# Optimization experiments

Measured on AMD Instinct MI355X. Metric: run time of the kernel, lower is better.

## Reference

```python
import jax, jax.numpy as jnp
import numpy as np

GRID = 256          # number of block rows/cols (shape[0] == shape[1])
BS = 256            # block size == shape[1] in SparseAdjacency
K = 3               # kernel_size (odd)
HK = K // 2
BATCH = 4
FEAT = 256


def _connectivity(bs, k):
    # banded binary matrix: ones on diagonals -k//2..k//2 (SparseAdjacency connectivity)
    c = jnp.zeros((bs, bs), dtype=jnp.float32)
    for d in range(-(k // 2), k // 2 + 1):
        c = c + jnp.diag(jnp.ones(bs - abs(d), dtype=jnp.float32), d)
    return c


def setup_inputs() -> dict:
    key = jax.random.key(0)
    x = jax.random.normal(key, (BATCH, GRID * BS, FEAT), dtype=jnp.float32)
    # SparseAdjacency stores K identical banded connectivity blocks
    conn = _connectivity(BS, K)
    blocks = jnp.stack([conn] * K, axis=0)  # [K, BS, BS]
    return {"x": x, "blocks": blocks}


def reference(x, blocks):
    # Block-banded BCSR matmul: out_block[i] = sum_{d=-HK..HK} blocks[d+HK] @ x_block[i+d]
    # (clipped at boundaries -> zero padding), exactly the ptr/indices/data pattern
    # built by SparseAdjacency and consumed by SemiRegSpraseBCSR.matmul.
    B, NNbs, F = x.shape
    k, bs, _ = blocks.shape
    hk = k // 2
    n = NNbs // bs
    xb = x.reshape(B, n, bs, F)
    out = jnp.zeros_like(xb)
    for d in range(-hk, hk + 1):
        if d >= 0:
            shifted = jnp.pad(xb[:, d:], ((0, 0), (0, d), (0, 0), (0, 0)))
        else:
            shifted = jnp.pad(xb[:, :d], ((0, 0), (-d, 0), (0, 0), (0, 0)))
        # [bs,bs] @ [B,n,bs,F] -> [B,n,bs,F]
        out = out + jnp.einsum('ij,bnjf->bnif', blocks[d + hk], shifted)
    return out.reshape(B, NNbs, F)
```

## Files before the change

kernel.cpp:

```cpp
#include <hip/hip_runtime.h>


#define NB   256
#define BS   256
#define F4   64
#define RPT  8
#define TY   4
#define ROWS_PER_WG (RPT * TY)
#define CHUNKS (BS / ROWS_PER_WG)

typedef float f32x4 __attribute__((ext_vector_type(4)));

__global__ __launch_bounds__(256)
void blockconv_kernel(const float* __restrict__ x,
                      const float* __restrict__ w,
                      float* __restrict__ out)
{
    const int tx = threadIdx.x;
    const int ty = threadIdx.y;
    const int wg = blockIdx.x;

    const int chunk = wg & (CHUNKS - 1);
    const int n     = (wg >> 3) & (NB - 1);
    const int b     = wg >> 11;

    const int i_base = chunk * ROWS_PER_WG + ty * RPT;
    const int jlo    = i_base - 1;
    const int jlo_cl = jlo < 0 ? 0 : jlo;
    const bool lo_ok = (jlo >= 0);
    const bool hi_ok = (jlo + RPT + 1) < BS;

    const f32x4* __restrict__ x4 = (const f32x4*)x;
    f32x4* __restrict__ out4     = (f32x4*)out;

    f32x4 acc[RPT];
#pragma unroll
    for (int i = 0; i < RPT; ++i) acc[i] = (f32x4)(0.f);

#pragma unroll
    for (int dd = 0; dd < 3; ++dd) {
        const int nn_raw = n + dd - 1;
        const bool d_ok  = (nn_raw >= 0) & (nn_raw < NB);
        const int  nn    = nn_raw < 0 ? 0 : (nn_raw >= NB ? NB - 1 : nn_raw);

        const f32x4* __restrict__ xblk = x4 + ((size_t)(b * NB + nn) * BS) * F4 + tx;
        const float* __restrict__  wblk = w + (size_t)dd * BS * BS;

        f32x4 v[RPT + 2];
        v[0] = xblk[(size_t)jlo_cl * F4];
#pragma unroll
        for (int jj = 1; jj <= RPT; ++jj)
            v[jj] = xblk[(size_t)(jlo + jj) * F4];
        v[RPT + 1] = xblk[(size_t)(hi_ok ? jlo + RPT + 1 : jlo + RPT) * F4];
        if (!lo_ok) v[0]       = (f32x4)(0.f);
        if (!hi_ok) v[RPT + 1] = (f32x4)(0.f);

        float wv[RPT][3];
#pragma unroll
        for (int ii = 0; ii < RPT; ++ii) {
            const int irow = i_base + ii;
#pragma unroll
            for (int c = 0; c < 3; ++c) {
                int j = irow - 1 + c;
                const bool j_ok = (j >= 0) & (j < BS);
                j = j < 0 ? 0 : (j >= BS ? BS - 1 : j);
                float raw = wblk[(size_t)irow * BS + j];
                raw = (d_ok & j_ok) ? raw : 0.f;
                const int bits = __builtin_amdgcn_readfirstlane(__float_as_int(raw));
                wv[ii][c] = __int_as_float(bits);
            }
        }

#pragma unroll
        for (int ii = 0; ii < RPT; ++ii) {
#pragma unroll
            for (int c = 0; c < 3; ++c) {
                const float s  = wv[ii][c];
                const f32x4 vv = v[ii + c];
                acc[ii].x = fmaf(s, vv.x, acc[ii].x);
                acc[ii].y = fmaf(s, vv.y, acc[ii].y);
                acc[ii].z = fmaf(s, vv.z, acc[ii].z);
                acc[ii].w = fmaf(s, vv.w, acc[ii].w);
            }
        }
    }

    const size_t obase = ((size_t)(b * NB + n) * BS + i_base) * F4 + tx;
#pragma unroll
    for (int i = 0; i < RPT; ++i)
        __builtin_nontemporal_store(acc[i], &out4[obase + (size_t)i * F4]);
}

extern "C" void kernel_launch(void* const* d_in, const int* in_sizes, int n_in,
                              void* d_out, int out_size, void* d_ws, size_t ws_size,
                              hipStream_t stream) {
    const float* x = (const float*)d_in[0];
    const float* w = (const float*)d_in[1];
    float* out = (float*)d_out;

    const int n_wg = 4 * NB * CHUNKS;
    dim3 block(64, TY);
    blockconv_kernel<<<n_wg, block, 0, stream>>>(x, w, out);
}
```

Measured before the change: 93.36 us.

## Stage banded weights in LDS and prefetch neighbor-block rows before FMAs

Each workgroup now loads its 32x3x3 banded weight coefficients once, cooperatively, into shared memory. This replaces the per-thread global weight reads that went through readfirstlane. The three neighbor-block x tiles are loaded up front with clamped row offsets, and their loads are interleaved with the FMA passes so memory latency overlaps with compute. Zero padding now comes from zeroed weights rather than zeroed data. In exchange the kernel adds a barrier and holds more vector registers live, which may lower occupancy in what is essentially a bandwidth-bound kernel.

```diff
diff --git a/kernel.cpp b/kernel.cpp
--- a/kernel.cpp
+++ b/kernel.cpp
@@ -8,6 +8,7 @@
 #define TY   4
 #define ROWS_PER_WG (RPT * TY)
 #define CHUNKS (BS / ROWS_PER_WG)
+#define NWG  (4 * NB * CHUNKS)
 
 typedef float f32x4 __attribute__((ext_vector_type(4)));
 
@@ -24,66 +25,86 @@
     const int n     = (wg >> 3) & (NB - 1);
     const int b     = wg >> 11;
 
+    __shared__ float wlds[ROWS_PER_WG][16];
+    {
+        const int tid = ty * 64 + tx;
+#pragma unroll
+        for (int e0 = 0; e0 < 2; ++e0) {
+            const int e  = tid + e0 * 256;
+            const int r  = e >> 4;
+            const int q  = e & 15;
+            const int dd = q >> 2;
+            const int c  = q & 3;
+            const int irow   = chunk * ROWS_PER_WG + r;
+            const int nn_raw = n + dd - 1;
+            int j = irow - 1 + c;
+            const bool ok = (dd < 3) & (c < 3) &
+                            (nn_raw >= 0) & (nn_raw < NB) &
+                            (j >= 0) & (j < BS);
+            j = j < 0 ? 0 : (j >= BS ? BS - 1 : j);
+            const int ddc = dd < 3 ? dd : 2;
+            const float raw = w[(size_t)ddc * BS * BS + (size_t)irow * BS + j];
+            wlds[r][q] = ok ? raw : 0.f;
+        }
+    }
+    __syncthreads();
+
     const int i_base = chunk * ROWS_PER_WG + ty * RPT;
     const int jlo    = i_base - 1;
-    const int jlo_cl = jlo < 0 ? 0 : jlo;
-    const bool lo_ok = (jlo >= 0);
-    const bool hi_ok = (jlo + RPT + 1) < BS;
 
     const f32x4* __restrict__ x4 = (const f32x4*)x;
     f32x4* __restrict__ out4     = (f32x4*)out;
+
+    const f32x4* xb[3];
+#pragma unroll
+    for (int dd = 0; dd < 3; ++dd) {
+        int nn = n + dd - 1;
+        nn = nn < 0 ? 0 : (nn >= NB ? NB - 1 : nn);
+        xb[dd] = x4 + ((size_t)(b * NB + nn) * BS) * F4 + tx;
+    }
 
     f32x4 acc[RPT];
 #pragma unroll
     for (int i = 0; i < RPT; ++i) acc[i] = (f32x4)(0.f);
 
+    size_t roff[RPT + 2];
 #pragma unroll
-    for (int dd = 0; dd < 3; ++dd) {
-        const int nn_raw = n + dd - 1;
-        const bool d_ok  = (nn_raw >= 0) & (nn_raw < NB);
-        const int  nn    = nn_raw < 0 ? 0 : (nn_raw >= NB ? NB - 1 : nn_raw);
+    for (int jj = 0; jj < RPT + 2; ++jj) {
+        int j = jlo + jj;
+        j = j < 0 ? 0 : (j >= BS ? BS - 1 : j);
+        roff[jj] = (size_t)j * F4;
+    }
 
-        const f32x4* __restrict__ xblk = x4 + ((size_t)(b * NB + nn) * BS) * F4 + tx;
-        const float* __restrict__  wblk = w + (size_t)dd * BS * BS;
+#define LOADW(V, DD)                                   \
+    _Pragma("unroll")                                  \
+    for (int jj = 0; jj < RPT + 2; ++jj)               \
+        V[jj] = xb[DD][roff[jj]];
 
-        f32x4 v[RPT + 2];
-        v[0] = xblk[(size_t)jlo_cl * F4];
-#pragma unroll
-        for (int jj = 1; jj <= RPT; ++jj)
-            v[jj] = xblk[(size_t)(jlo + jj) * F4];
-        v[RPT + 1] = xblk[(size_t)(hi_ok ? jlo + RPT + 1 : jlo + RPT) * F4];
-        if (!lo_ok) v[0]       = (f32x4)(0.f);
-        if (!hi_ok) v[RPT + 1] = (f32x4)(0.f);
+#define FMAW(V, DD)                                            \
+    _Pragma("unroll")                                          \
+    for (int ii = 0; ii < RPT; ++ii) {                         \
+        const f32x4 wr = *(const f32x4*)&wlds[ty * RPT + ii][(DD) * 4]; \
+        _Pragma("unroll")                                      \
+        for (int c = 0; c < 3; ++c) {                          \
+            const float s  = wr[c];                            \
+            const f32x4 vv = V[ii + c];                        \
+            acc[ii].x = fmaf(s, vv.x, acc[ii].x);              \
+            acc[ii].y = fmaf(s, vv.y, acc[ii].y);              \
+            acc[ii].z = fmaf(s, vv.z, acc[ii].z);              \
+            acc[ii].w = fmaf(s, vv.w, acc[ii].w);              \
+        }                                                      \
+    }
 
-        float wv[RPT][3];
-#pragma unroll
-        for (int ii = 0; ii < RPT; ++ii) {
-            const int irow = i_base + ii;
-#pragma unroll
-            for (int c = 0; c < 3; ++c) {
-                int j = irow - 1 + c;
-                const bool j_ok = (j >= 0) & (j < BS);
-                j = j < 0 ? 0 : (j >= BS ? BS - 1 : j);
-                float raw = wblk[(size_t)irow * BS + j];
-                raw = (d_ok & j_ok) ? raw : 0.f;
-                const int bits = __builtin_amdgcn_readfirstlane(__float_as_int(raw));
-                wv[ii][c] = __int_as_float(bits);
-            }
-        }
+    f32x4 v0[RPT + 2], v1[RPT + 2], v2[RPT + 2];
+    LOADW(v0, 0)
+    LOADW(v1, 1)
+    FMAW(v0, 0)
+    LOADW(v2, 2)
+    FMAW(v1, 1)
+    FMAW(v2, 2)
 
-#pragma unroll
-        for (int ii = 0; ii < RPT; ++ii) {
-#pragma unroll
-            for (int c = 0; c < 3; ++c) {
-                const float s  = wv[ii][c];
-                const f32x4 vv = v[ii + c];
-                acc[ii].x = fmaf(s, vv.x, acc[ii].x);
-                acc[ii].y = fmaf(s, vv.y, acc[ii].y);
-                acc[ii].z = fmaf(s, vv.z, acc[ii].z);
-                acc[ii].w = fmaf(s, vv.w, acc[ii].w);
-            }
-        }
-    }
+#undef LOADW
+#undef FMAW
 
     const size_t obase = ((size_t)(b * NB + n) * BS + i_base) * F4 + tx;
 #pragma unroll
@@ -98,7 +119,6 @@
     const float* w = (const float*)d_in[1];
     float* out = (float*)d_out;
 
-    const int n_wg = 4 * NB * CHUNKS;
     dim3 block(64, TY);
-    blockconv_kernel<<<n_wg, block, 0, stream>>>(x, w, out);
+    blockconv_kernel<<<NWG, block, 0, stream>>>(x, w, out);
 }
```

Result: faster. 83.91 us (-10.1%).
